# Kernel tuning notes

Measured on AMD Instinct MI355X. Metric: run time of the kernel, lower is better.

The kernel has to match this reference:

```python
import jax, jax.numpy as jnp
import numpy as np

N, E, FEAT, C, H, D, L, T, MS, MD, NC = 20000, 320000, 128, 256, 8, 32, 5, 64, 10, 128, 2
NEG_SLOPE = 0.2


def setup_inputs() -> dict:
    key = jax.random.key(0)
    ks = jax.random.split(key, 20)
    g = lambda k, shape, fan: jax.random.normal(k, shape, jnp.float32) / np.sqrt(fan)
    return {
        "x_initial_nodes": jax.random.normal(ks[0], (N, FEAT), jnp.float32),
        "edge_index": jax.random.randint(ks[1], (2, E), 0, N, jnp.int32),
        "time_embedding": jax.random.normal(ks[2], (N, T), jnp.float32),
        "Wi": g(ks[3], (FEAT, C), FEAT),
        "bi": jnp.zeros((C,), jnp.float32),
        "Wg": g(ks[4], (L, C, C), C),          # GAT projection per layer
        "a_src": g(ks[5], (L, H, D), D),        # attention vectors
        "a_dst": g(ks[6], (L, H, D), D),
        "Wt": g(ks[7], (L, T, C), T),           # time-embedding fusion
        "Wq": g(ks[8], (L, C, C), C),           # memory cross-attention
        "Wk": g(ks[9], (L, MD, C), MD),
        "Wv": g(ks[10], (L, MD, C), MD),
        "global_memory": jax.random.normal(ks[11], (MS, MD), jnp.float32),
        "Wc": g(ks[12], (C + MD, NC), C + MD),
        "bc": jnp.zeros((NC,), jnp.float32),
    }


def _stm_layer(x, src, dst, t_proj, mem, Wg, a_s, a_d, Wq, Wk, Wv):
    # GAT-style message passing with time fusion
    h = ((x + t_proj) @ Wg).reshape(N, H, D)                      # [N,H,D]
    e_src = jnp.einsum('nhd,hd->nh', h, a_s)                      # [N,H]
    e_dst = jnp.einsum('nhd,hd->nh', h, a_d)
    logits = jax.nn.leaky_relu(e_src[src] + e_dst[dst], NEG_SLOPE)  # [E,H]
    m = jax.ops.segment_max(logits, dst, num_segments=N)
    m = jnp.where(jnp.isfinite(m), m, 0.0)                        # empty segments
    ex = jnp.exp(logits - m[dst])
    denom = jax.ops.segment_sum(ex, dst, num_segments=N)
    alpha = ex / (denom[dst] + 1e-16)                             # [E,H]
    msg = jax.ops.segment_sum(alpha[:, :, None] * h[src], dst, num_segments=N)
    node = jax.nn.relu(msg.reshape(N, C))
    # cross-attention to global memory bank
    q = node @ Wq                                                  # [N,C]
    k = mem @ Wk                                                   # [MS,C]
    v = mem @ Wv                                                   # [MS,C]
    attn = jax.nn.softmax(q @ k.T / np.sqrt(C), axis=-1)           # [N,MS]
    return jax.nn.relu(node + attn @ v + x)                        # residual


def reference(x_initial_nodes, edge_index, time_embedding, Wi, bi, Wg, a_src,
              a_dst, Wt, Wq, Wk, Wv, global_memory, Wc, bc):
    src, dst = edge_index[0], edge_index[1]
    node = jax.nn.relu(x_initial_nodes @ Wi + bi)                  # [N,C]
    for l in range(L):
        t_proj = time_embedding @ Wt[l]                            # [N,C]
        node = _stm_layer(node, src, dst, t_proj, global_memory,
                          Wg[l], a_src[l], a_dst[l], Wq[l], Wk[l], Wv[l])
    pooled = jnp.mean(node, axis=0)                                # [C]
    mem_pooled = jnp.mean(global_memory, axis=0)                   # [MD]
    final = jnp.concatenate([pooled, mem_pooled], axis=-1)         # [C+MD]
    return final @ Wc + bc                                         # [NC]
```

## Files before the change

kernel.cpp:

```cpp
#include <hip/hip_runtime.h>
#include <hip/hip_bf16.h>

#define N_NODES 20000
#define E_EDGES 320000
#define FEAT 128
#define CDIM 256
#define NHEAD 8
#define HDIM 32
#define NLAYER 5
#define TDIM 64
#define MSLOT 10
#define MDIM 128
#define NCLS 2

typedef unsigned short ushort_t;
typedef short short8 __attribute__((ext_vector_type(8)));
typedef float floatx4 __attribute__((ext_vector_type(4)));

__device__ __forceinline__ ushort_t f2bf(float f) {
    union { float f; unsigned int u; } t; t.f = f;
    unsigned int r = (t.u + 0x7FFF + ((t.u >> 16) & 1)) >> 16;
    return (ushort_t)r;
}
__device__ __forceinline__ float bf2f(ushort_t u) {
    union { float f; unsigned int u; } t; t.u = ((unsigned int)u) << 16;
    return t.f;
}

__global__ __launch_bounds__(256) void gemm_mfma(
    const ushort_t* __restrict__ A1, int lda1, int K1,
    const ushort_t* __restrict__ A2, int lda2, int Ktot,
    const ushort_t* __restrict__ Bt,
    const float* __restrict__ bias,
    ushort_t* Cbf, int doRelu, int M)
{
    __shared__ __align__(16) ushort_t smemA[64 * 32];
    __shared__ __align__(16) ushort_t smemB[128 * 32];
    int tid = threadIdx.x;
    int lane = tid & 63, wid = tid >> 6;
    int li = lane & 15, lq = lane >> 4;
    int row0 = blockIdx.y * 64;
    int col0 = blockIdx.x * 128;

    floatx4 acc[4][2];
#pragma unroll
    for (int a = 0; a < 4; a++)
#pragma unroll
        for (int b = 0; b < 2; b++) acc[a][b] = {0.f, 0.f, 0.f, 0.f};

    int ar = tid >> 2, ac = tid & 3;
    int agc = (ac - (ar >> 1)) & 3;
    int arow = row0 + ar; if (arow >= M) arow = M - 1;

    for (int k0 = 0; k0 < Ktot; k0 += 32) {
        __syncthreads();
        const ushort_t* Ab; int lda;
        if (k0 < K1) { Ab = A1 + k0; lda = lda1; }
        else         { Ab = A2 + (k0 - K1); lda = lda2; }
        {
            const void* g = (const void*)(Ab + (size_t)arow * lda + agc * 8);
            __builtin_amdgcn_global_load_lds(
                (const __attribute__((address_space(1))) void*)g,
                (__attribute__((address_space(3))) void*)&smemA[wid * 512], 16, 0, 0);
        }
#pragma unroll
        for (int j = 0; j < 2; j++) {
            int slot = j * 256 + tid;
            int n = slot >> 2, c = slot & 3;
            int gc = (c - (n >> 1)) & 3;
            const void* g = (const void*)(Bt + (size_t)(col0 + n) * Ktot + k0 + gc * 8);
            __builtin_amdgcn_global_load_lds(
                (const __attribute__((address_space(1))) void*)g,
                (__attribute__((address_space(3))) void*)&smemB[(j * 256 + wid * 64) * 8], 16, 0, 0);
        }
        __syncthreads();

        short8 af[4], bfr[2];
#pragma unroll
        for (int mt = 0; mt < 4; mt++) {
            int m = mt * 16 + li;
            int sw = (lq + (m >> 1)) & 3;
            af[mt] = *(const short8*)&smemA[m * 32 + sw * 8];
        }
#pragma unroll
        for (int nt = 0; nt < 2; nt++) {
            int nl = wid * 32 + nt * 16 + li;
            int sw = (lq + (nl >> 1)) & 3;
            bfr[nt] = *(const short8*)&smemB[nl * 32 + sw * 8];
        }
#pragma unroll
        for (int mt = 0; mt < 4; mt++)
#pragma unroll
            for (int nt = 0; nt < 2; nt++)
                acc[mt][nt] = __builtin_amdgcn_mfma_f32_16x16x32_bf16(af[mt], bfr[nt], acc[mt][nt], 0, 0, 0);
    }

#pragma unroll
    for (int mt = 0; mt < 4; mt++) {
        int row = row0 + mt * 16 + lq * 4;
#pragma unroll
        for (int nt = 0; nt < 2; nt++) {
            int col = col0 + wid * 32 + nt * 16 + li;
            float bv = bias ? bias[col] : 0.f;
#pragma unroll
            for (int r = 0; r < 4; r++) {
                if (row + r < M) {
                    float v = acc[mt][nt][r] + bv;
                    if (doRelu) v = fmaxf(v, 0.f);
                    Cbf[(size_t)(row + r) * CDIM + col] = f2bf(v);
                }
            }
        }
    }
}

__global__ __launch_bounds__(256) void gemm_h(
    const ushort_t* __restrict__ A1, int lda1, int K1,
    const ushort_t* __restrict__ A2, int lda2, int Ktot,
    const ushort_t* __restrict__ Bt,
    const float* __restrict__ a_s, const float* __restrict__ a_d,
    ushort_t* __restrict__ Cbf,
    float* __restrict__ esrc, float* __restrict__ edst, int M)
{
    __shared__ __align__(16) ushort_t smemA[64 * 32];
    __shared__ __align__(16) ushort_t smemB[128 * 32];
    int tid = threadIdx.x;
    int lane = tid & 63, wid = tid >> 6;
    int li = lane & 15, lq = lane >> 4;
    int row0 = blockIdx.y * 64;
    int col0 = blockIdx.x * 128;

    floatx4 acc[4][2];
#pragma unroll
    for (int a = 0; a < 4; a++)
#pragma unroll
        for (int b = 0; b < 2; b++) acc[a][b] = {0.f, 0.f, 0.f, 0.f};

    int ar = tid >> 2, ac = tid & 3;
    int agc = (ac - (ar >> 1)) & 3;
    int arow = row0 + ar; if (arow >= M) arow = M - 1;

    for (int k0 = 0; k0 < Ktot; k0 += 32) {
        __syncthreads();
        const ushort_t* Ab; int lda;
        if (k0 < K1) { Ab = A1 + k0; lda = lda1; }
        else         { Ab = A2 + (k0 - K1); lda = lda2; }
        {
            const void* g = (const void*)(Ab + (size_t)arow * lda + agc * 8);
            __builtin_amdgcn_global_load_lds(
                (const __attribute__((address_space(1))) void*)g,
                (__attribute__((address_space(3))) void*)&smemA[wid * 512], 16, 0, 0);
        }
#pragma unroll
        for (int j = 0; j < 2; j++) {
            int slot = j * 256 + tid;
            int n = slot >> 2, c = slot & 3;
            int gc = (c - (n >> 1)) & 3;
            const void* g = (const void*)(Bt + (size_t)(col0 + n) * Ktot + k0 + gc * 8);
            __builtin_amdgcn_global_load_lds(
                (const __attribute__((address_space(1))) void*)g,
                (__attribute__((address_space(3))) void*)&smemB[(j * 256 + wid * 64) * 8], 16, 0, 0);
        }
        __syncthreads();

        short8 af[4], bfr[2];
#pragma unroll
        for (int mt = 0; mt < 4; mt++) {
            int m = mt * 16 + li;
            int sw = (lq + (m >> 1)) & 3;
            af[mt] = *(const short8*)&smemA[m * 32 + sw * 8];
        }
#pragma unroll
        for (int nt = 0; nt < 2; nt++) {
            int nl = wid * 32 + nt * 16 + li;
            int sw = (lq + (nl >> 1)) & 3;
            bfr[nt] = *(const short8*)&smemB[nl * 32 + sw * 8];
        }
#pragma unroll
        for (int mt = 0; mt < 4; mt++)
#pragma unroll
            for (int nt = 0; nt < 2; nt++)
                acc[mt][nt] = __builtin_amdgcn_mfma_f32_16x16x32_bf16(af[mt], bfr[nt], acc[mt][nt], 0, 0, 0);
    }

    int hd = blockIdx.x * 4 + wid;
    float as0 = a_s[col0 + wid * 32 + li];
    float as1 = a_s[col0 + wid * 32 + 16 + li];
    float ad0 = a_d[col0 + wid * 32 + li];
    float ad1 = a_d[col0 + wid * 32 + 16 + li];

#pragma unroll
    for (int mt = 0; mt < 4; mt++) {
        int row = row0 + mt * 16 + lq * 4;
#pragma unroll
        for (int nt = 0; nt < 2; nt++) {
            int col = col0 + wid * 32 + nt * 16 + li;
#pragma unroll
            for (int r = 0; r < 4; r++)
                if (row + r < M)
                    Cbf[(size_t)(row + r) * CDIM + col] = f2bf(acc[mt][nt][r]);
        }
#pragma unroll
        for (int r = 0; r < 4; r++) {
            float ps = acc[mt][0][r] * as0 + acc[mt][1][r] * as1;
            float pd = acc[mt][0][r] * ad0 + acc[mt][1][r] * ad1;
#pragma unroll
            for (int d = 1; d < 16; d <<= 1) {
                ps += __shfl_xor(ps, d);
                pd += __shfl_xor(pd, d);
            }
            if (li == 0 && row + r < M) {
                esrc[(size_t)(row + r) * NHEAD + hd] = ps;
                edst[(size_t)(row + r) * NHEAD + hd] = pd;
            }
        }
    }
}

__global__ __launch_bounds__(256) void gemm64(
    const float* __restrict__ A, const float* __restrict__ A2,
    const float* __restrict__ B, const float* __restrict__ bias,
    float* __restrict__ C, int M, int K, int Nf, int doRelu,
    int sA, int sB, int sC)
{
    __shared__ float As[16][64];
    __shared__ float Bs[16][64];
    A += (size_t)blockIdx.z * sA;
    B += (size_t)blockIdx.z * sB;
    C += (size_t)blockIdx.z * sC;
    int tid = threadIdx.x;
    int tx = tid & 15, ty = tid >> 4;
    int row0 = blockIdx.y * 64, col0 = blockIdx.x * 64;
    int ar = tid >> 2;
    int ac = (tid & 3) * 4;

    float acc[4][4] = {};

    for (int k0 = 0; k0 < K; k0 += 16) {
        int arow = row0 + ar;
        float4 av = make_float4(0.f, 0.f, 0.f, 0.f);
        if (arow < M) {
            av = *(const float4*)(A + (size_t)arow * K + k0 + ac);
            if (A2) {
                float4 a2 = *(const float4*)(A2 + (size_t)arow * K + k0 + ac);
                av.x += a2.x; av.y += a2.y; av.z += a2.z; av.w += a2.w;
            }
        }
        As[ac + 0][ar] = av.x;
        As[ac + 1][ar] = av.y;
        As[ac + 2][ar] = av.z;
        As[ac + 3][ar] = av.w;
        float4 bv = *(const float4*)(B + (size_t)(k0 + (tid >> 4)) * Nf + col0 + (tid & 15) * 4);
        *(float4*)&Bs[tid >> 4][(tid & 15) * 4] = bv;
        __syncthreads();
#pragma unroll
        for (int kk = 0; kk < 16; kk++) {
            float4 a = *(const float4*)&As[kk][ty * 4];
            float4 b = *(const float4*)&Bs[kk][tx * 4];
            acc[0][0] += a.x * b.x; acc[0][1] += a.x * b.y; acc[0][2] += a.x * b.z; acc[0][3] += a.x * b.w;
            acc[1][0] += a.y * b.x; acc[1][1] += a.y * b.y; acc[1][2] += a.y * b.z; acc[1][3] += a.y * b.w;
            acc[2][0] += a.z * b.x; acc[2][1] += a.z * b.y; acc[2][2] += a.z * b.z; acc[2][3] += a.z * b.w;
            acc[3][0] += a.w * b.x; acc[3][1] += a.w * b.y; acc[3][2] += a.w * b.z; acc[3][3] += a.w * b.w;
        }
        __syncthreads();
    }

    float4 bv = make_float4(0.f, 0.f, 0.f, 0.f);
    if (bias) bv = *(const float4*)(bias + col0 + tx * 4);
#pragma unroll
    for (int i = 0; i < 4; i++) {
        int r = row0 + ty * 4 + i;
        if (r < M) {
            float4 o;
            o.x = acc[i][0] + bv.x;
            o.y = acc[i][1] + bv.y;
            o.z = acc[i][2] + bv.z;
            o.w = acc[i][3] + bv.w;
            if (doRelu) {
                o.x = fmaxf(o.x, 0.f); o.y = fmaxf(o.y, 0.f);
                o.z = fmaxf(o.z, 0.f); o.w = fmaxf(o.w, 0.f);
            }
            *(float4*)(C + (size_t)r * Nf + col0 + tx * 4) = o;
        }
    }
}

__global__ void cvt_bf16(const float* __restrict__ in, ushort_t* __restrict__ out, int n)
{
    int i = blockIdx.x * blockDim.x + threadIdx.x;
    if (i < n) out[i] = f2bf(in[i]);
}

__global__ __launch_bounds__(256) void transpose_cast(
    const float* __restrict__ in, int K, int Nn,
    ushort_t* __restrict__ out, int ostride, int koff,
    int inBatchStride, int outBatchStride)
{
    __shared__ float tile[32][33];
    in  += (size_t)blockIdx.z * inBatchStride;
    out += (size_t)blockIdx.z * outBatchStride;
    int k0 = blockIdx.y * 32, n0 = blockIdx.x * 32;
    int tx = threadIdx.x & 31, ty = threadIdx.x >> 5;
#pragma unroll
    for (int j = 0; j < 4; j++)
        tile[ty + j * 8][tx] = in[(size_t)(k0 + ty + j * 8) * Nn + n0 + tx];
    __syncthreads();
#pragma unroll
    for (int j = 0; j < 4; j++) {
        int n = n0 + ty + j * 8;
        out[(size_t)n * ostride + koff + k0 + tx] = f2bf(tile[tx][ty + j * 8]);
    }
}

__global__ __launch_bounds__(256) void wqk_build(
    const float* __restrict__ Wq, const float* __restrict__ kbufs,
    float* __restrict__ wqk)
{
    int j = blockIdx.x, l = blockIdx.y;
    int d = threadIdx.x;
    __shared__ float kk[CDIM];
    kk[d] = kbufs[((size_t)l * MSLOT + j) * CDIM + d];
    __syncthreads();
    const float* wrow = Wq + ((size_t)l * CDIM + d) * CDIM;
    float acc = 0.f;
#pragma unroll 4
    for (int c = 0; c < CDIM; c++) acc += wrow[c] * kk[c];
    wqk[((size_t)l * MSLOT + j) * CDIM + d] = acc * 0.0625f;
}

__global__ void count_deg(const int* __restrict__ dst, int* __restrict__ deg, int ne)
{
    int e = blockIdx.x * blockDim.x + threadIdx.x;
    if (e < ne) atomicAdd(&deg[dst[e]], 1);
}

__global__ __launch_bounds__(1024) void scan_kernel(const int* __restrict__ deg,
                                                    int* __restrict__ offs, int n)
{
    __shared__ int swt[16];
    int tid = threadIdx.x, lane = tid & 63, wid = tid >> 6;
    int base = tid * 20;
    int v[20];
    int s = 0;
#pragma unroll
    for (int i = 0; i < 20; i++) {
        int d = (base + i < n) ? deg[base + i] : 0;
        v[i] = d; s += d;
    }
    int x = s;
#pragma unroll
    for (int d = 1; d < 64; d <<= 1) {
        int t = __shfl_up(x, d);
        if (lane >= d) x += t;
    }
    if (lane == 63) swt[wid] = x;
    __syncthreads();
    if (wid == 0) {
        int w = (lane < 16) ? swt[lane] : 0;
#pragma unroll
        for (int d = 1; d < 16; d <<= 1) {
            int t = __shfl_up(w, d);
            if (lane >= d) w += t;
        }
        if (lane < 16) swt[lane] = w;
    }
    __syncthreads();
    int wbase = (wid == 0) ? 0 : swt[wid - 1];
    int run = wbase + x - s;
#pragma unroll
    for (int i = 0; i < 20; i++) {
        if (base + i < n) offs[base + i] = run;
        run += v[i];
    }
}

__global__ void fill_csr(const int* __restrict__ src, const int* __restrict__ dst,
                         const int* __restrict__ offs, int* __restrict__ cursor,
                         int* __restrict__ csr_src, int ne)
{
    int e = blockIdx.x * blockDim.x + threadIdx.x;
    if (e < ne) {
        int d = dst[e];
        int p = atomicAdd(&cursor[d], 1);
        csr_src[offs[d] + p] = src[e];
    }
}

__global__ __launch_bounds__(256) void gat_agg_fused(
    const ushort_t* __restrict__ h, const float* __restrict__ esrc, const float* __restrict__ edst,
    const int* __restrict__ offs, const int* __restrict__ deg, const int* __restrict__ csr_src,
    const float* __restrict__ wqk, const float* __restrict__ vbuf,
    const ushort_t* __restrict__ node_in,
    ushort_t* __restrict__ node_out, int n)
{
    int tid = threadIdx.x;
    int lane = tid & 63;
    int wslot = tid >> 6;
    int node = blockIdx.x * 4 + wslot;
    int start = offs[node], cnt = deg[node];
    int chead = lane >> 3;

    float4 gat4;
    if (cnt <= 64) {
        int eh = lane >> 3, hh = lane & 7;
        float edl = edst[(size_t)node * NHEAD + hh];
        int sl = (lane < cnt) ? csr_src[start + lane] : 0;
        int nit = (cnt + 7) >> 3;
        float lg[8], w8[8];
        float m = -3.0e38f;
#pragma unroll
        for (int it = 0; it < 8; it++) {
            float v = -3.0e38f;
            if (it < nit) {
                int e = it * 8 + eh;
                int se = __shfl(sl, e);
                if (e < cnt) {
                    float t = esrc[(size_t)se * NHEAD + hh] + edl;
                    v = t > 0.f ? t : 0.2f * t;
                }
            }
            lg[it] = v;
            m = fmaxf(m, v);
        }
        m = fmaxf(m, __shfl_xor(m, 8));
        m = fmaxf(m, __shfl_xor(m, 16));
        m = fmaxf(m, __shfl_xor(m, 32));
        float den = 0.f;
#pragma unroll
        for (int it = 0; it < 8; it++) {
            float w = 0.f;
            if (it < nit) {
                int e = it * 8 + eh;
                if (e < cnt) w = __expf(lg[it] - m);
            }
            w8[it] = w;
            den += w;
        }
        den += __shfl_xor(den, 8);
        den += __shfl_xor(den, 16);
        den += __shfl_xor(den, 32);
        float inv = 1.f / (den + 1e-16f);
        float invc = __shfl(inv, chead);

        float4 acc = make_float4(0.f, 0.f, 0.f, 0.f);
#pragma unroll
        for (int rr = 0; rr < 8; rr++) {
            if (rr < nit) {
                int sv[8]; float av[8];
#pragma unroll
                for (int k = 0; k < 8; k++) {
                    sv[k] = __shfl(sl, rr * 8 + k);
                    av[k] = __shfl(w8[rr], (k << 3) | chead);
                }
                ushort4 hv[8];
#pragma unroll
                for (int k = 0; k < 8; k++)
                    hv[k] = *(const ushort4*)(h + (size_t)sv[k] * CDIM + lane * 4);
#pragma unroll
                for (int k = 0; k < 8; k++) {
                    acc.x += av[k] * bf2f(hv[k].x);
                    acc.y += av[k] * bf2f(hv[k].y);
                    acc.z += av[k] * bf2f(hv[k].z);
                    acc.w += av[k] * bf2f(hv[k].w);
                }
            }
        }
        gat4.x = fmaxf(acc.x * invc, 0.f);
        gat4.y = fmaxf(acc.y * invc, 0.f);
        gat4.z = fmaxf(acc.z * invc, 0.f);
        gat4.w = fmaxf(acc.w * invc, 0.f);
    } else {
        int hh = lane & 7;
        float edl = edst[(size_t)node * NHEAD + hh];
        float m = -3.0e38f;
        int i8 = lane >> 3;
        for (int i = 0; i < cnt; i += 8) {
            int ii = i + i8;
            if (ii < cnt) {
                int s = csr_src[start + ii];
                float lgv = esrc[(size_t)s * NHEAD + hh] + edl;
                lgv = lgv > 0.f ? lgv : 0.2f * lgv;
                m = fmaxf(m, lgv);
            }
        }
        m = fmaxf(m, __shfl_xor(m, 8));
        m = fmaxf(m, __shfl_xor(m, 16));
        m = fmaxf(m, __shfl_xor(m, 32));
        float4 acc = make_float4(0.f, 0.f, 0.f, 0.f);
        float den = 0.f;
        for (int i = 0; i < cnt; i++) {
            int s = csr_src[start + i];
            float lgv = esrc[(size_t)s * NHEAD + hh] + edl;
            lgv = lgv > 0.f ? lgv : 0.2f * lgv;
            float w = __expf(lgv - m);
            den += w;
            float wc = __shfl(w, chead);
            ushort4 hu = *(const ushort4*)(h + (size_t)s * CDIM + lane * 4);
            acc.x += wc * bf2f(hu.x); acc.y += wc * bf2f(hu.y);
            acc.z += wc * bf2f(hu.z); acc.w += wc * bf2f(hu.w);
        }
        float dc = __shfl(den, chead) + 1e-16f;
        float inv = 1.f / dc;
        gat4.x = fmaxf(acc.x * inv, 0.f);
        gat4.y = fmaxf(acc.y * inv, 0.f);
        gat4.z = fmaxf(acc.z * inv, 0.f);
        gat4.w = fmaxf(acc.w * inv, 0.f);
    }

    float s[MSLOT];
#pragma unroll
    for (int j = 0; j < MSLOT; j++) {
        float4 w4 = *(const float4*)(wqk + j * CDIM + lane * 4);
        s[j] = gat4.x * w4.x + gat4.y * w4.y + gat4.z * w4.z + gat4.w * w4.w;
    }
#pragma unroll
    for (int d = 1; d < 64; d <<= 1) {
#pragma unroll
        for (int j = 0; j < MSLOT; j++) s[j] += __shfl_xor(s[j], d);
    }
    float m = s[0];
#pragma unroll
    for (int j = 1; j < MSLOT; j++) m = fmaxf(m, s[j]);
    float sum = 0.f;
#pragma unroll
    for (int j = 0; j < MSLOT; j++) { s[j] = __expf(s[j] - m); sum += s[j]; }
    float inv = 1.f / sum;

    ushort4 c4 = *(const ushort4*)(node_in + (size_t)node * CDIM + lane * 4);
    float4 o;
    o.x = gat4.x + bf2f(c4.x); o.y = gat4.y + bf2f(c4.y);
    o.z = gat4.z + bf2f(c4.z); o.w = gat4.w + bf2f(c4.w);
#pragma unroll
    for (int j = 0; j < MSLOT; j++) {
        float p = s[j] * inv;
        float4 v4 = *(const float4*)(vbuf + j * CDIM + lane * 4);
        o.x += p * v4.x; o.y += p * v4.y; o.z += p * v4.z; o.w += p * v4.w;
    }
    o.x = fmaxf(o.x, 0.f); o.y = fmaxf(o.y, 0.f); o.z = fmaxf(o.z, 0.f); o.w = fmaxf(o.w, 0.f);
    ushort4 ob;
    ob.x = f2bf(o.x); ob.y = f2bf(o.y); ob.z = f2bf(o.z); ob.w = f2bf(o.w);
    *(ushort4*)(node_out + (size_t)node * CDIM + lane * 4) = ob;
}

__global__ void col_sum(const ushort_t* __restrict__ node, float* __restrict__ pooled, int n)
{
    float acc = 0.f;
    int c = threadIdx.x;
    for (int r = blockIdx.x; r < n; r += gridDim.x) acc += bf2f(node[(size_t)r * CDIM + c]);
    atomicAdd(&pooled[c], acc);
}

__global__ void finalize(const float* __restrict__ pooled, const float* __restrict__ mem,
                         const float* __restrict__ Wc, const float* __restrict__ bc,
                         float* __restrict__ out)
{
    int lane = threadIdx.x;
    float a0 = 0.f, a1 = 0.f;
    for (int i = lane; i < CDIM + MDIM; i += 64) {
        float f;
        if (i < CDIM) {
            f = pooled[i] * (1.0f / (float)N_NODES);
        } else {
            float s = 0.f;
            for (int r = 0; r < MSLOT; r++) s += mem[r * MDIM + (i - CDIM)];
            f = s * (1.0f / (float)MSLOT);
        }
        a0 += f * Wc[i * NCLS + 0];
        a1 += f * Wc[i * NCLS + 1];
    }
#pragma unroll
    for (int d = 1; d < 64; d <<= 1) { a0 += __shfl_xor(a0, d); a1 += __shfl_xor(a1, d); }
    if (lane == 0) { out[0] = a0 + bc[0]; out[1] = a1 + bc[1]; }
}

extern "C" void kernel_launch(void* const* d_in, const int* in_sizes, int n_in,
                              void* d_out, int out_size, void* d_ws, size_t ws_size,
                              hipStream_t stream)
{
    const float* x    = (const float*)d_in[0];
    const int*   ei   = (const int*)d_in[1];
    const float* temb = (const float*)d_in[2];
    const float* Wi   = (const float*)d_in[3];
    const float* bi   = (const float*)d_in[4];
    const float* Wg   = (const float*)d_in[5];
    const float* a_s  = (const float*)d_in[6];
    const float* a_d  = (const float*)d_in[7];
    const float* Wt   = (const float*)d_in[8];
    const float* Wq   = (const float*)d_in[9];
    const float* Wk   = (const float*)d_in[10];
    const float* Wv   = (const float*)d_in[11];
    const float* mem  = (const float*)d_in[12];
    const float* Wc   = (const float*)d_in[13];
    const float* bc   = (const float*)d_in[14];
    float* out = (float*)d_out;
    char* ws = (char*)d_ws;

    const size_t NCB_BYTES = (size_t)N_NODES * CDIM * 2;
    size_t off = 0;
    ushort_t* nodeA  = (ushort_t*)(ws + off); off += NCB_BYTES;
    ushort_t* nodeB  = (ushort_t*)(ws + off); off += NCB_BYTES;
    ushort_t* hbf    = (ushort_t*)(ws + off); off += NCB_BYTES;
    ushort_t* xbf    = (ushort_t*)(ws + off); off += (size_t)N_NODES * FEAT * 2;
    ushort_t* tembbf = (ushort_t*)(ws + off); off += (size_t)N_NODES * TDIM * 2;
    float* esrc   = (float*)(ws + off); off += (size_t)N_NODES * NHEAD * 4;
    float* edst   = (float*)(ws + off); off += (size_t)N_NODES * NHEAD * 4;
    float* kbufs  = (float*)(ws + off); off += (size_t)NLAYER * MSLOT * CDIM * 4;
    float* vbufs  = (float*)(ws + off); off += (size_t)NLAYER * MSLOT * CDIM * 4;
    float* wqkL   = (float*)(ws + off); off += (size_t)NLAYER * MSLOT * CDIM * 4;
    float* Wtp    = (float*)(ws + off); off += (size_t)NLAYER * TDIM * CDIM * 4;
    ushort_t* Bt_i = (ushort_t*)(ws + off); off += (size_t)CDIM * FEAT * 2;
    ushort_t* Bt_h = (ushort_t*)(ws + off); off += (size_t)NLAYER * CDIM * (CDIM + TDIM) * 2;
    size_t zero_base = off;
    float* pooled = (float*)(ws + off); off += CDIM * 4;
    int* deg      = (int*)(ws + off);   off += N_NODES * 4;
    int* cursor   = (int*)(ws + off);   off += N_NODES * 4;
    size_t zero_len = off - zero_base;
    int* offs     = (int*)(ws + off);   off += (N_NODES + 4) * 4;
    int* csr_src  = (int*)(ws + off);   off += (size_t)E_EDGES * 4;

    const int* srcIdx = ei;
    const int* dstIdx = ei + E_EDGES;

    hipMemsetAsync(ws + zero_base, 0, zero_len, stream);

    cvt_bf16<<<(N_NODES * FEAT + 255) / 256, 256, 0, stream>>>(x, xbf, N_NODES * FEAT);
    cvt_bf16<<<(N_NODES * TDIM + 255) / 256, 256, 0, stream>>>(temb, tembbf, N_NODES * TDIM);
    gemm64<<<dim3(4, 1, NLAYER), 256, 0, stream>>>(Wt, nullptr, Wg, nullptr, Wtp,
        TDIM, CDIM, CDIM, 0, TDIM * CDIM, CDIM * CDIM, TDIM * CDIM);
    transpose_cast<<<dim3(CDIM / 32, FEAT / 32, 1), 256, 0, stream>>>(
        Wi, FEAT, CDIM, Bt_i, FEAT, 0, 0, 0);
    transpose_cast<<<dim3(CDIM / 32, CDIM / 32, NLAYER), 256, 0, stream>>>(
        Wg, CDIM, CDIM, Bt_h, CDIM + TDIM, 0, CDIM * CDIM, CDIM * (CDIM + TDIM));
    transpose_cast<<<dim3(CDIM / 32, TDIM / 32, NLAYER), 256, 0, stream>>>(
        Wtp, TDIM, CDIM, Bt_h, CDIM + TDIM, CDIM, TDIM * CDIM, CDIM * (CDIM + TDIM));
    gemm64<<<dim3(4, 1, NLAYER), 256, 0, stream>>>(mem, nullptr, Wk, nullptr, kbufs,
        MSLOT, MDIM, CDIM, 0, 0, MDIM * CDIM, MSLOT * CDIM);
    gemm64<<<dim3(4, 1, NLAYER), 256, 0, stream>>>(mem, nullptr, Wv, nullptr, vbufs,
        MSLOT, MDIM, CDIM, 0, 0, MDIM * CDIM, MSLOT * CDIM);
    wqk_build<<<dim3(MSLOT, NLAYER), 256, 0, stream>>>(Wq, kbufs, wqkL);

    count_deg<<<(E_EDGES + 255) / 256, 256, 0, stream>>>(dstIdx, deg, E_EDGES);
    scan_kernel<<<1, 1024, 0, stream>>>(deg, offs, N_NODES);
    fill_csr<<<(E_EDGES + 255) / 256, 256, 0, stream>>>(srcIdx, dstIdx, offs, cursor, csr_src, E_EDGES);

    dim3 mfmaGrid(2, (N_NODES + 63) / 64);
    int nodeBlocks = N_NODES / 4;

    gemm_mfma<<<mfmaGrid, 256, 0, stream>>>(xbf, FEAT, FEAT, nullptr, 0, FEAT,
                                            Bt_i, bi, nodeA, 1, N_NODES);

    ushort_t* cur = nodeA;
    ushort_t* alt = nodeB;
    for (int l = 0; l < NLAYER; l++) {
        gemm_h<<<mfmaGrid, 256, 0, stream>>>(cur, CDIM, CDIM, tembbf, TDIM, CDIM + TDIM,
                                             Bt_h + (size_t)l * CDIM * (CDIM + TDIM),
                                             a_s + (size_t)l * CDIM, a_d + (size_t)l * CDIM,
                                             hbf, esrc, edst, N_NODES);
        gat_agg_fused<<<nodeBlocks, 256, 0, stream>>>(hbf, esrc, edst, offs, deg, csr_src,
                                                      wqkL + (size_t)l * MSLOT * CDIM,
                                                      vbufs + (size_t)l * MSLOT * CDIM,
                                                      cur, alt, N_NODES);
        ushort_t* t = cur; cur = alt; alt = t;
    }

    col_sum<<<128, 256, 0, stream>>>(cur, pooled, N_NODES);
    finalize<<<1, 64, 0, stream>>>(pooled, mem, Wc, bc, out);
}
```

Measured before the change: 508.3 us.

## Store GAT projections as FP8 and shrink GEMM row tile to 32

```diff
diff --git a/kernel.cpp b/kernel.cpp
--- a/kernel.cpp
+++ b/kernel.cpp
@@ -14,8 +14,10 @@
 #define NCLS 2
 
 typedef unsigned short ushort_t;
+typedef unsigned char uchar_t;
 typedef short short8 __attribute__((ext_vector_type(8)));
 typedef float floatx4 __attribute__((ext_vector_type(4)));
+typedef float floatx2 __attribute__((ext_vector_type(2)));
 
 __device__ __forceinline__ ushort_t f2bf(float f) {
     union { float f; unsigned int u; } t; t.f = f;
@@ -32,33 +34,32 @@
     const ushort_t* __restrict__ A2, int lda2, int Ktot,
     const ushort_t* __restrict__ Bt,
     const float* __restrict__ bias,
-    ushort_t* Cbf, int doRelu, int M)
-{
-    __shared__ __align__(16) ushort_t smemA[64 * 32];
+    ushort_t* Cbf, int doRelu)
+{
+    __shared__ __align__(16) ushort_t smemA[32 * 32];
     __shared__ __align__(16) ushort_t smemB[128 * 32];
     int tid = threadIdx.x;
     int lane = tid & 63, wid = tid >> 6;
     int li = lane & 15, lq = lane >> 4;
-    int row0 = blockIdx.y * 64;
+    int row0 = blockIdx.y * 32;
     int col0 = blockIdx.x * 128;
 
-    floatx4 acc[4][2];
-#pragma unroll
-    for (int a = 0; a < 4; a++)
+    floatx4 acc[2][2];
+#pragma unroll
+    for (int a = 0; a < 2; a++)
 #pragma unroll
         for (int b = 0; b < 2; b++) acc[a][b] = {0.f, 0.f, 0.f, 0.f};
 
     int ar = tid >> 2, ac = tid & 3;
     int agc = (ac - (ar >> 1)) & 3;
-    int arow = row0 + ar; if (arow >= M) arow = M - 1;
 
     for (int k0 = 0; k0 < Ktot; k0 += 32) {
         __syncthreads();
         const ushort_t* Ab; int lda;
         if (k0 < K1) { Ab = A1 + k0; lda = lda1; }
         else         { Ab = A2 + (k0 - K1); lda = lda2; }
-        {
-            const void* g = (const void*)(Ab + (size_t)arow * lda + agc * 8);
+        if (wid < 2) {
+            const void* g = (const void*)(Ab + (size_t)(row0 + ar) * lda + agc * 8);
             __builtin_amdgcn_global_load_lds(
                 (const __attribute__((address_space(1))) void*)g,
                 (__attribute__((address_space(3))) void*)&smemA[wid * 512], 16, 0, 0);
@@ -75,9 +76,9 @@
         }
         __syncthreads();
 
-        short8 af[4], bfr[2];
-#pragma unroll
-        for (int mt = 0; mt < 4; mt++) {
+        short8 af[2], bfr[2];
+#pragma unroll
+        for (int mt = 0; mt < 2; mt++) {
             int m = mt * 16 + li;
             int sw = (lq + (m >> 1)) & 3;
             af[mt] = *(const short8*)&smemA[m * 32 + sw * 8];
@@ -89,14 +90,14 @@
             bfr[nt] = *(const short8*)&smemB[nl * 32 + sw * 8];
         }
 #pragma unroll
-        for (int mt = 0; mt < 4; mt++)
+        for (int mt = 0; mt < 2; mt++)
 #pragma unroll
             for (int nt = 0; nt < 2; nt++)
                 acc[mt][nt] = __builtin_amdgcn_mfma_f32_16x16x32_bf16(af[mt], bfr[nt], acc[mt][nt], 0, 0, 0);
     }
 
 #pragma unroll
-    for (int mt = 0; mt < 4; mt++) {
+    for (int mt = 0; mt < 2; mt++) {
         int row = row0 + mt * 16 + lq * 4;
 #pragma unroll
         for (int nt = 0; nt < 2; nt++) {
@@ -104,11 +105,9 @@
             float bv = bias ? bias[col] : 0.f;
 #pragma unroll
             for (int r = 0; r < 4; r++) {
-                if (row + r < M) {
-                    float v = acc[mt][nt][r] + bv;
-                    if (doRelu) v = fmaxf(v, 0.f);
-                    Cbf[(size_t)(row + r) * CDIM + col] = f2bf(v);
-                }
+                float v = acc[mt][nt][r] + bv;
+                if (doRelu) v = fmaxf(v, 0.f);
+                Cbf[(size_t)(row + r) * CDIM + col] = f2bf(v);
             }
         }
     }
@@ -119,34 +118,33 @@
     const ushort_t* __restrict__ A2, int lda2, int Ktot,
     const ushort_t* __restrict__ Bt,
     const float* __restrict__ a_s, const float* __restrict__ a_d,
-    ushort_t* __restrict__ Cbf,
-    float* __restrict__ esrc, float* __restrict__ edst, int M)
-{
-    __shared__ __align__(16) ushort_t smemA[64 * 32];
+    uchar_t* __restrict__ Cf8,
+    float* __restrict__ esrc, float* __restrict__ edst)
+{
+    __shared__ __align__(16) ushort_t smemA[32 * 32];
     __shared__ __align__(16) ushort_t smemB[128 * 32];
     int tid = threadIdx.x;
     int lane = tid & 63, wid = tid >> 6;
     int li = lane & 15, lq = lane >> 4;
-    int row0 = blockIdx.y * 64;
+    int row0 = blockIdx.y * 32;
     int col0 = blockIdx.x * 128;
 
-    floatx4 acc[4][2];
-#pragma unroll
-    for (int a = 0; a < 4; a++)
+    floatx4 acc[2][2];
+#pragma unroll
+    for (int a = 0; a < 2; a++)
 #pragma unroll
         for (int b = 0; b < 2; b++) acc[a][b] = {0.f, 0.f, 0.f, 0.f};
 
     int ar = tid >> 2, ac = tid & 3;
     int agc = (ac - (ar >> 1)) & 3;
-    int arow = row0 + ar; if (arow >= M) arow = M - 1;
 
     for (int k0 = 0; k0 < Ktot; k0 += 32) {
         __syncthreads();
         const ushort_t* Ab; int lda;
         if (k0 < K1) { Ab = A1 + k0; lda = lda1; }
         else         { Ab = A2 + (k0 - K1); lda = lda2; }
-        {
-            const void* g = (const void*)(Ab + (size_t)arow * lda + agc * 8);
+        if (wid < 2) {
+            const void* g = (const void*)(Ab + (size_t)(row0 + ar) * lda + agc * 8);
             __builtin_amdgcn_global_load_lds(
                 (const __attribute__((address_space(1))) void*)g,
                 (__attribute__((address_space(3))) void*)&smemA[wid * 512], 16, 0, 0);
@@ -163,9 +161,9 @@
         }
         __syncthreads();
 
-        short8 af[4], bfr[2];
-#pragma unroll
-        for (int mt = 0; mt < 4; mt++) {
+        short8 af[2], bfr[2];
+#pragma unroll
+        for (int mt = 0; mt < 2; mt++) {
             int m = mt * 16 + li;
             int sw = (lq + (m >> 1)) & 3;
             af[mt] = *(const short8*)&smemA[m * 32 + sw * 8];
@@ -177,39 +175,37 @@
             bfr[nt] = *(const short8*)&smemB[nl * 32 + sw * 8];
         }
 #pragma unroll
-        for (int mt = 0; mt < 4; mt++)
+        for (int mt = 0; mt < 2; mt++)
 #pragma unroll
             for (int nt = 0; nt < 2; nt++)
                 acc[mt][nt] = __builtin_amdgcn_mfma_f32_16x16x32_bf16(af[mt], bfr[nt], acc[mt][nt], 0, 0, 0);
     }
 
     int hd = blockIdx.x * 4 + wid;
-    float as0 = a_s[col0 + wid * 32 + li];
-    float as1 = a_s[col0 + wid * 32 + 16 + li];
-    float ad0 = a_d[col0 + wid * 32 + li];
-    float ad1 = a_d[col0 + wid * 32 + 16 + li];
-
-#pragma unroll
-    for (int mt = 0; mt < 4; mt++) {
+    int cbase = col0 + wid * 32 + li;
+    float as0 = a_s[cbase];
+    float as1 = a_s[cbase + 16];
+    float ad0 = a_d[cbase];
+    float ad1 = a_d[cbase + 16];
+
+#pragma unroll
+    for (int mt = 0; mt < 2; mt++) {
         int row = row0 + mt * 16 + lq * 4;
 #pragma unroll
-        for (int nt = 0; nt < 2; nt++) {
-            int col = col0 + wid * 32 + nt * 16 + li;
-#pragma unroll
-            for (int r = 0; r < 4; r++)
-                if (row + r < M)
-                    Cbf[(size_t)(row + r) * CDIM + col] = f2bf(acc[mt][nt][r]);
-        }
-#pragma unroll
         for (int r = 0; r < 4; r++) {
-            float ps = acc[mt][0][r] * as0 + acc[mt][1][r] * as1;
-            float pd = acc[mt][0][r] * ad0 + acc[mt][1][r] * ad1;
+            float v0 = acc[mt][0][r];
+            float v1 = acc[mt][1][r];
+            unsigned int pk = __builtin_amdgcn_cvt_pk_fp8_f32(v0, v1, 0, false);
+            Cf8[(size_t)(row + r) * CDIM + cbase]      = (uchar_t)(pk & 0xff);
+            Cf8[(size_t)(row + r) * CDIM + cbase + 16] = (uchar_t)((pk >> 8) & 0xff);
+            float ps = v0 * as0 + v1 * as1;
+            float pd = v0 * ad0 + v1 * ad1;
 #pragma unroll
             for (int d = 1; d < 16; d <<= 1) {
                 ps += __shfl_xor(ps, d);
                 pd += __shfl_xor(pd, d);
             }
-            if (li == 0 && row + r < M) {
+            if (li == 0) {
                 esrc[(size_t)(row + r) * NHEAD + hd] = ps;
                 edst[(size_t)(row + r) * NHEAD + hd] = pd;
             }
@@ -387,7 +383,7 @@
 }
 
 __global__ __launch_bounds__(256) void gat_agg_fused(
-    const ushort_t* __restrict__ h, const float* __restrict__ esrc, const float* __restrict__ edst,
+    const uchar_t* __restrict__ h, const float* __restrict__ esrc, const float* __restrict__ edst,
     const int* __restrict__ offs, const int* __restrict__ deg, const int* __restrict__ csr_src,
     const float* __restrict__ wqk, const float* __restrict__ vbuf,
     const ushort_t* __restrict__ node_in,
@@ -452,16 +448,18 @@
                     sv[k] = __shfl(sl, rr * 8 + k);
                     av[k] = __shfl(w8[rr], (k << 3) | chead);
                 }
-                ushort4 hv[8];
+                unsigned int hw[8];
 #pragma unroll
                 for (int k = 0; k < 8; k++)
-                    hv[k] = *(const ushort4*)(h + (size_t)sv[k] * CDIM + lane * 4);
+                    hw[k] = *(const unsigned int*)(h + (size_t)sv[k] * CDIM + lane * 4);
 #pragma unroll
                 for (int k = 0; k < 8; k++) {
-                    acc.x += av[k] * bf2f(hv[k].x);
-                    acc.y += av[k] * bf2f(hv[k].y);
-                    acc.z += av[k] * bf2f(hv[k].z);
-                    acc.w += av[k] * bf2f(hv[k].w);
+                    floatx2 lo = __builtin_amdgcn_cvt_pk_f32_fp8((int)hw[k], false);
+                    floatx2 hi = __builtin_amdgcn_cvt_pk_f32_fp8((int)hw[k], true);
+                    acc.x += av[k] * lo.x;
+                    acc.y += av[k] * lo.y;
+                    acc.z += av[k] * hi.x;
+                    acc.w += av[k] * hi.y;
                 }
             }
         }
@@ -495,9 +493,11 @@
             float w = __expf(lgv - m);
             den += w;
             float wc = __shfl(w, chead);
-            ushort4 hu = *(const ushort4*)(h + (size_t)s * CDIM + lane * 4);
-            acc.x += wc * bf2f(hu.x); acc.y += wc * bf2f(hu.y);
-            acc.z += wc * bf2f(hu.z); acc.w += wc * bf2f(hu.w);
+            unsigned int hwv = *(const unsigned int*)(h + (size_t)s * CDIM + lane * 4);
+            floatx2 lo = __builtin_amdgcn_cvt_pk_f32_fp8((int)hwv, false);
+            floatx2 hi = __builtin_amdgcn_cvt_pk_f32_fp8((int)hwv, true);
+            acc.x += wc * lo.x; acc.y += wc * lo.y;
+            acc.z += wc * hi.x; acc.w += wc * hi.y;
         }
         float dc = __shfl(den, chead) + 1e-16f;
         float inv = 1.f / dc;
@@ -599,7 +599,7 @@
     size_t off = 0;
     ushort_t* nodeA  = (ushort_t*)(ws + off); off += NCB_BYTES;
     ushort_t* nodeB  = (ushort_t*)(ws + off); off += NCB_BYTES;
-    ushort_t* hbf    = (ushort_t*)(ws + off); off += NCB_BYTES;
+    uchar_t*  hf8    = (uchar_t*)(ws + off);  off += (size_t)N_NODES * CDIM;
     ushort_t* xbf    = (ushort_t*)(ws + off); off += (size_t)N_NODES * FEAT * 2;
     ushort_t* tembbf = (ushort_t*)(ws + off); off += (size_t)N_NODES * TDIM * 2;
     float* esrc   = (float*)(ws + off); off += (size_t)N_NODES * NHEAD * 4;
@@ -643,11 +643,11 @@
     scan_kernel<<<1, 1024, 0, stream>>>(deg, offs, N_NODES);
     fill_csr<<<(E_EDGES + 255) / 256, 256, 0, stream>>>(srcIdx, dstIdx, offs, cursor, csr_src, E_EDGES);
 
-    dim3 mfmaGrid(2, (N_NODES + 63) / 64);
+    dim3 mfmaGrid(2, N_NODES / 32);
     int nodeBlocks = N_NODES / 4;
 
     gemm_mfma<<<mfmaGrid, 256, 0, stream>>>(xbf, FEAT, FEAT, nullptr, 0, FEAT,
-                                            Bt_i, bi, nodeA, 1, N_NODES);
+                                            Bt_i, bi, nodeA, 1);
 
     ushort_t* cur = nodeA;
     ushort_t* alt = nodeB;
@@ -655,8 +655,8 @@
         gemm_h<<<mfmaGrid, 256, 0, stream>>>(cur, CDIM, CDIM, tembbf, TDIM, CDIM + TDIM,
                                              Bt_h + (size_t)l * CDIM * (CDIM + TDIM),
                                              a_s + (size_t)l * CDIM, a_d + (size_t)l * CDIM,
-                                             hbf, esrc, edst, N_NODES);
-        gat_agg_fused<<<nodeBlocks, 256, 0, stream>>>(hbf, esrc, edst, offs, deg, csr_src,
+                                             hf8, esrc, edst);
+        gat_agg_fused<<<nodeBlocks, 256, 0, stream>>>(hf8, esrc, edst, offs, deg, csr_src,
                                                       wqkL + (size_t)l * MSLOT * CDIM,
                                                       vbufs + (size_t)l * MSLOT * CDIM,
                                                       cur, alt, N_NODES);
```

New measurement: 479.2 us. 1.06x faster.
